# Optimization experiments

Measured on AMD Instinct MI355X. Metric: run time of the kernel, lower is better.

## Reference

```python
import jax, jax.numpy as jnp
import numpy as np

D_MODEL = 1024
HEADS = 4
HDIM = 64


def setup_inputs() -> dict:
    key = jax.random.key(0)
    k_x, k_qw, k_qb, k_kw, k_kb, k_hw = jax.random.split(key, 6)
    hidden_states = jax.random.normal(k_x, (2, 4096, D_MODEL), dtype=jnp.float32)
    # xavier_uniform bound for Linear(d_model -> heads*hdim)
    fan_out = HEADS * HDIM
    bound = float(np.sqrt(6.0 / (D_MODEL + fan_out)))
    q_weight = jax.random.uniform(k_qw, (fan_out, D_MODEL), minval=-bound, maxval=bound, dtype=jnp.float32)
    k_weight = jax.random.uniform(k_kw, (fan_out, D_MODEL), minval=-bound, maxval=bound, dtype=jnp.float32)
    # nn.Linear default bias init: U(-1/sqrt(fan_in), 1/sqrt(fan_in))
    b_bound = float(1.0 / np.sqrt(D_MODEL))
    q_bias = jax.random.uniform(k_qb, (fan_out,), minval=-b_bound, maxval=b_bound, dtype=jnp.float32)
    k_bias = jax.random.uniform(k_kb, (fan_out,), minval=-b_bound, maxval=b_bound, dtype=jnp.float32)
    indexer_weights = jax.random.normal(k_hw, (HEADS,), dtype=jnp.float32) * 0.1
    return {
        "hidden_states": hidden_states,
        "q_weight": q_weight,
        "q_bias": q_bias,
        "k_weight": k_weight,
        "k_bias": k_bias,
        "indexer_weights": indexer_weights,
    }


def reference(hidden_states, q_weight, q_bias, k_weight, k_bias, indexer_weights):
    b, s, _ = hidden_states.shape
    # Linear projections: x @ W^T + b  -> [b, s, heads*hdim]
    q = hidden_states @ q_weight.T + q_bias
    k = hidden_states @ k_weight.T + k_bias
    q = q.reshape(b, s, HEADS, HDIM)  # [b, s, h, d]
    k = k.reshape(b, s, HEADS, HDIM)
    # per-head QK^T -> [b, h, s, s]
    scores = jnp.einsum("bqhd,bkhd->bhqk", q, k)
    scores = jax.nn.relu(scores)
    # weighted sum over heads -> [b, s, s]
    index_scores = jnp.einsum("bhqk,h->bqk", scores, indexer_weights)
    return index_scores
```

## Files before the change

### kernel.cpp

```cpp
#include <hip/hip_runtime.h>


typedef __bf16 bf16;
typedef __bf16 bf16x4 __attribute__((ext_vector_type(4)));
typedef __bf16 bf16x8 __attribute__((ext_vector_type(8)));
typedef float f32x4 __attribute__((ext_vector_type(4)));

#define NB 2
#define SEQ 4096
#define DMODEL 1024
#define NHEAD 4
#define HDIM 64
#define NPROJ 256
#define MTOT 8192

__device__ __forceinline__ void async16(const void* g, void* l) {
  __builtin_amdgcn_global_load_lds(
      (const __attribute__((address_space(1))) void*)g,
      (__attribute__((address_space(3))) void*)l, 16, 0, 0);
}

__global__ __launch_bounds__(256) void k_convert(const float* __restrict__ wq,
                                                 const float* __restrict__ wk,
                                                 bf16* __restrict__ wqb,
                                                 bf16* __restrict__ wkb) {
  int i = blockIdx.x * 256 + threadIdx.x;
  float4 a = ((const float4*)wq)[i];
  bf16x4 oa = {(bf16)a.x, (bf16)a.y, (bf16)a.z, (bf16)a.w};
  ((bf16x4*)wqb)[i] = oa;
  float4 b = ((const float4*)wk)[i];
  bf16x4 ob = {(bf16)b.x, (bf16)b.y, (bf16)b.z, (bf16)b.w};
  ((bf16x4*)wkb)[i] = ob;
}

__global__ __launch_bounds__(256, 3) void k_proj(
    const float* __restrict__ x, const bf16* __restrict__ wqb,
    const bf16* __restrict__ wkb, const float* __restrict__ qbias,
    const float* __restrict__ kbias, bf16* __restrict__ Qb,
    bf16* __restrict__ Kb) {
  __shared__ __align__(16) bf16 As[64 * 72];
  __shared__ __align__(16) bf16 Bs[256 * 64];
  const int t = threadIdx.x;
  const int lane = t & 63, w = t >> 6;
  const int m16 = lane & 15, q = lane >> 4;
  const int m0 = blockIdx.x * 64;
  const int z = blockIdx.y;
  const bf16* W = z ? wkb : wqb;

  f32x4 acc[4][4];
#pragma unroll
  for (int i = 0; i < 4; i++)
#pragma unroll
    for (int j = 0; j < 4; j++) acc[i][j] = {0.f, 0.f, 0.f, 0.f};

  for (int kt = 0; kt < 16; kt++) {
#pragma unroll
    for (int p = 0; p < 8; p++) {
      int n0 = p * 32 + w * 8;
      int r = n0 + (lane >> 3);
      int c = (lane & 7) ^ (r & 7);
      async16(W + (size_t)r * DMODEL + kt * 64 + c * 8, Bs + n0 * 64);
    }
#pragma unroll
    for (int p = 0; p < 4; p++) {
      int r = p * 16 + (t >> 4);
      int c = (t & 15) * 4;
      float4 v = *(const float4*)(x + (size_t)(m0 + r) * DMODEL + kt * 64 + c);
      bf16x4 o = {(bf16)v.x, (bf16)v.y, (bf16)v.z, (bf16)v.w};
      *(bf16x4*)(As + r * 72 + c) = o;
    }
    __builtin_amdgcn_s_waitcnt(0);
    __syncthreads();

#pragma unroll
    for (int s = 0; s < 2; s++) {
      bf16x8 a[4], b[4];
#pragma unroll
      for (int mt = 0; mt < 4; mt++)
        a[mt] = *(const bf16x8*)(As + (mt * 16 + m16) * 72 + s * 32 + q * 8);
#pragma unroll
      for (int nt = 0; nt < 4; nt++) {
        int n = w * 64 + nt * 16 + m16;
        int cc = (4 * s + q) ^ (n & 7);
        b[nt] = *(const bf16x8*)(Bs + n * 64 + cc * 8);
      }
#pragma unroll
      for (int mt = 0; mt < 4; mt++)
#pragma unroll
        for (int nt = 0; nt < 4; nt++)
          acc[mt][nt] = __builtin_amdgcn_mfma_f32_16x16x32_bf16(
              a[mt], b[nt], acc[mt][nt], 0, 0, 0);
    }
    __syncthreads();
  }

  const float* bias = z ? kbias : qbias;
  bf16* outp = z ? Kb : Qb;
#pragma unroll
  for (int nt = 0; nt < 4; nt++) {
    int col = w * 64 + nt * 16 + m16;
    float bv = bias[col];
#pragma unroll
    for (int mt = 0; mt < 4; mt++) {
      int row0 = m0 + mt * 16 + q * 4;
#pragma unroll
      for (int e = 0; e < 4; e++)
        outp[(size_t)(row0 + e) * NPROJ + col] = (bf16)(acc[mt][nt][e] + bv);
    }
  }
}

__global__ __launch_bounds__(256, 2) void k_scores(
    const bf16* __restrict__ Qb, const bf16* __restrict__ Kb,
    const float* __restrict__ iw, float* __restrict__ out) {
  __shared__ __align__(16) bf16 Qs[128 * 64];
  __shared__ __align__(16) bf16 Ks[128 * 64];
  const int t = threadIdx.x;
  const int lane = t & 63, w = t >> 6;
  const int m16 = lane & 15, q = lane >> 4;
  const int kx = blockIdx.x, qy = blockIdx.y, bz = blockIdx.z;
  const int rh = (w >> 1) * 64, ch = (w & 1) * 64;

  f32x4 accf[4][4];
#pragma unroll
  for (int i = 0; i < 4; i++)
#pragma unroll
    for (int j = 0; j < 4; j++) accf[i][j] = {0.f, 0.f, 0.f, 0.f};

  const size_t qbase = ((size_t)bz * SEQ + (size_t)qy * 128) * NPROJ;
  const size_t kbase = ((size_t)bz * SEQ + (size_t)kx * 128) * NPROJ;

  for (int h = 0; h < NHEAD; h++) {
#pragma unroll
    for (int p = 0; p < 4; p++) {
      int r0 = w * 32 + p * 8;
      int r = r0 + (lane >> 3);
      int c = (lane & 7) ^ (r & 7);
      async16(Qb + qbase + (size_t)r * NPROJ + h * 64 + c * 8, Qs + r0 * 64);
      async16(Kb + kbase + (size_t)r * NPROJ + h * 64 + c * 8, Ks + r0 * 64);
    }
    __builtin_amdgcn_s_waitcnt(0);
    __syncthreads();

    float wh = iw[h];
    bf16x8 b0[4], b1[4];
#pragma unroll
    for (int nt = 0; nt < 4; nt++) {
      int n = ch + nt * 16 + m16;
      b0[nt] = *(const bf16x8*)(Ks + n * 64 + ((q) ^ (n & 7)) * 8);
      b1[nt] = *(const bf16x8*)(Ks + n * 64 + ((4 + q) ^ (n & 7)) * 8);
    }
#pragma unroll
    for (int mt = 0; mt < 4; mt++) {
      int m = rh + mt * 16 + m16;
      bf16x8 a0 = *(const bf16x8*)(Qs + m * 64 + ((q) ^ (m & 7)) * 8);
      bf16x8 a1 = *(const bf16x8*)(Qs + m * 64 + ((4 + q) ^ (m & 7)) * 8);
#pragma unroll
      for (int nt = 0; nt < 4; nt++) {
        f32x4 tacc = {0.f, 0.f, 0.f, 0.f};
        tacc = __builtin_amdgcn_mfma_f32_16x16x32_bf16(a0, b0[nt], tacc, 0, 0, 0);
        tacc = __builtin_amdgcn_mfma_f32_16x16x32_bf16(a1, b1[nt], tacc, 0, 0, 0);
#pragma unroll
        for (int e = 0; e < 4; e++)
          accf[mt][nt][e] += wh * fmaxf(tacc[e], 0.f);
      }
    }
    __syncthreads();
  }

#pragma unroll
  for (int mt = 0; mt < 4; mt++)
#pragma unroll
    for (int e = 0; e < 4; e++) {
      int row = qy * 128 + rh + mt * 16 + q * 4 + e;
      size_t ob = ((size_t)bz * SEQ + row) * SEQ + (size_t)kx * 128 + ch;
#pragma unroll
      for (int nt = 0; nt < 4; nt++)
        out[ob + nt * 16 + m16] = accf[mt][nt][e];
    }
}

extern "C" void kernel_launch(void* const* d_in, const int* in_sizes, int n_in,
                              void* d_out, int out_size, void* d_ws, size_t ws_size,
                              hipStream_t stream) {
  const float* x  = (const float*)d_in[0];
  const float* wq = (const float*)d_in[1];
  const float* qb = (const float*)d_in[2];
  const float* wk = (const float*)d_in[3];
  const float* kb = (const float*)d_in[4];
  const float* iw = (const float*)d_in[5];
  float* out = (float*)d_out;

  char* ws = (char*)d_ws;
  bf16* wqb = (bf16*)ws;
  bf16* wkb = (bf16*)(ws + 524288);
  bf16* Qb  = (bf16*)(ws + 1048576);
  bf16* Kb  = (bf16*)(ws + 1048576 + 4194304);

  k_convert<<<256, 256, 0, stream>>>(wq, wk, wqb, wkb);
  k_proj<<<dim3(128, 2, 1), 256, 0, stream>>>(x, wqb, wkb, qb, kb, Qb, Kb);
  k_scores<<<dim3(32, 32, 2), 256, 0, stream>>>(Qb, Kb, iw, out);
}
```

Measured before the change: 201.3 us.

## Drop LDS staging; load MFMA operands directly from global in proj and scores

Both the projection and the scores kernels stop staging tiles in shared memory and instead load MFMA fragments straight from global memory into registers, which removes the barriers and LDS traffic. The projection tile shrinks to 32 rows per block, giving twice as many blocks, and occupancy hints rise for both kernels. In exchange, operands that were shared across waves are now re-read by each wave through the caches, and loads are less coalesced.

```diff
diff --git a/kernel.cpp b/kernel.cpp
--- a/kernel.cpp
+++ b/kernel.cpp
@@ -14,12 +14,6 @@
 #define NPROJ 256
 #define MTOT 8192
 
-__device__ __forceinline__ void async16(const void* g, void* l) {
-  __builtin_amdgcn_global_load_lds(
-      (const __attribute__((address_space(1))) void*)g,
-      (__attribute__((address_space(3))) void*)l, 16, 0, 0);
-}
-
 __global__ __launch_bounds__(256) void k_convert(const float* __restrict__ wq,
                                                  const float* __restrict__ wk,
                                                  bf16* __restrict__ wqb,
@@ -33,75 +27,63 @@
   ((bf16x4*)wkb)[i] = ob;
 }
 
-__global__ __launch_bounds__(256, 3) void k_proj(
+__global__ __launch_bounds__(256, 4) void k_proj(
     const float* __restrict__ x, const bf16* __restrict__ wqb,
     const bf16* __restrict__ wkb, const float* __restrict__ qbias,
     const float* __restrict__ kbias, bf16* __restrict__ Qb,
     bf16* __restrict__ Kb) {
-  __shared__ __align__(16) bf16 As[64 * 72];
-  __shared__ __align__(16) bf16 Bs[256 * 64];
   const int t = threadIdx.x;
   const int lane = t & 63, w = t >> 6;
   const int m16 = lane & 15, q = lane >> 4;
-  const int m0 = blockIdx.x * 64;
+  const int m0 = blockIdx.x * 32;
   const int z = blockIdx.y;
-  const bf16* W = z ? wkb : wqb;
+  const bf16* __restrict__ W = z ? wkb : wqb;
 
-  f32x4 acc[4][4];
+  f32x4 acc[2][4];
 #pragma unroll
-  for (int i = 0; i < 4; i++)
+  for (int i = 0; i < 2; i++)
 #pragma unroll
     for (int j = 0; j < 4; j++) acc[i][j] = {0.f, 0.f, 0.f, 0.f};
 
+  const float* xp = x + (size_t)(m0 + m16) * DMODEL + q * 8;
+  const bf16* wp = W + (size_t)(w * 64 + m16) * DMODEL + q * 8;
+
   for (int kt = 0; kt < 16; kt++) {
+    bf16x8 a[2][2];
 #pragma unroll
-    for (int p = 0; p < 8; p++) {
-      int n0 = p * 32 + w * 8;
-      int r = n0 + (lane >> 3);
-      int c = (lane & 7) ^ (r & 7);
-      async16(W + (size_t)r * DMODEL + kt * 64 + c * 8, Bs + n0 * 64);
-    }
+    for (int mt = 0; mt < 2; mt++)
 #pragma unroll
-    for (int p = 0; p < 4; p++) {
-      int r = p * 16 + (t >> 4);
-      int c = (t & 15) * 4;
-      float4 v = *(const float4*)(x + (size_t)(m0 + r) * DMODEL + kt * 64 + c);
-      bf16x4 o = {(bf16)v.x, (bf16)v.y, (bf16)v.z, (bf16)v.w};
-      *(bf16x4*)(As + r * 72 + c) = o;
-    }
-    __builtin_amdgcn_s_waitcnt(0);
-    __syncthreads();
-
+      for (int s = 0; s < 2; s++) {
+        const float* p = xp + (size_t)mt * 16 * DMODEL + kt * 64 + s * 32;
+        float4 v0 = *(const float4*)p;
+        float4 v1 = *(const float4*)(p + 4);
+        a[mt][s] = bf16x8{(bf16)v0.x, (bf16)v0.y, (bf16)v0.z, (bf16)v0.w,
+                          (bf16)v1.x, (bf16)v1.y, (bf16)v1.z, (bf16)v1.w};
+      }
+    bf16x8 b[4][2];
 #pragma unroll
-    for (int s = 0; s < 2; s++) {
-      bf16x8 a[4], b[4];
+    for (int nt = 0; nt < 4; nt++)
 #pragma unroll
-      for (int mt = 0; mt < 4; mt++)
-        a[mt] = *(const bf16x8*)(As + (mt * 16 + m16) * 72 + s * 32 + q * 8);
+      for (int s = 0; s < 2; s++)
+        b[nt][s] = *(const bf16x8*)(wp + (size_t)nt * 16 * DMODEL + kt * 64 + s * 32);
 #pragma unroll
-      for (int nt = 0; nt < 4; nt++) {
-        int n = w * 64 + nt * 16 + m16;
-        int cc = (4 * s + q) ^ (n & 7);
-        b[nt] = *(const bf16x8*)(Bs + n * 64 + cc * 8);
-      }
+    for (int mt = 0; mt < 2; mt++)
 #pragma unroll
-      for (int mt = 0; mt < 4; mt++)
+      for (int nt = 0; nt < 4; nt++)
 #pragma unroll
-        for (int nt = 0; nt < 4; nt++)
+        for (int s = 0; s < 2; s++)
           acc[mt][nt] = __builtin_amdgcn_mfma_f32_16x16x32_bf16(
-              a[mt], b[nt], acc[mt][nt], 0, 0, 0);
-    }
-    __syncthreads();
+              a[mt][s], b[nt][s], acc[mt][nt], 0, 0, 0);
   }
 
-  const float* bias = z ? kbias : qbias;
-  bf16* outp = z ? Kb : Qb;
+  const float* __restrict__ bias = z ? kbias : qbias;
+  bf16* __restrict__ outp = z ? Kb : Qb;
 #pragma unroll
   for (int nt = 0; nt < 4; nt++) {
     int col = w * 64 + nt * 16 + m16;
     float bv = bias[col];
 #pragma unroll
-    for (int mt = 0; mt < 4; mt++) {
+    for (int mt = 0; mt < 2; mt++) {
       int row0 = m0 + mt * 16 + q * 4;
 #pragma unroll
       for (int e = 0; e < 4; e++)
@@ -110,11 +92,9 @@
   }
 }
 
-__global__ __launch_bounds__(256, 2) void k_scores(
+__global__ __launch_bounds__(256, 3) void k_scores(
     const bf16* __restrict__ Qb, const bf16* __restrict__ Kb,
     const float* __restrict__ iw, float* __restrict__ out) {
-  __shared__ __align__(16) bf16 Qs[128 * 64];
-  __shared__ __align__(16) bf16 Ks[128 * 64];
   const int t = threadIdx.x;
   const int lane = t & 63, w = t >> 6;
   const int m16 = lane & 15, q = lane >> 4;
@@ -127,45 +107,36 @@
 #pragma unroll
     for (int j = 0; j < 4; j++) accf[i][j] = {0.f, 0.f, 0.f, 0.f};
 
-  const size_t qbase = ((size_t)bz * SEQ + (size_t)qy * 128) * NPROJ;
-  const size_t kbase = ((size_t)bz * SEQ + (size_t)kx * 128) * NPROJ;
+  const float w0 = iw[0], w1 = iw[1], w2 = iw[2], w3 = iw[3];
+  const float whs[4] = {w0, w1, w2, w3};
+
+  const bf16* qp = Qb + (size_t)(bz * SEQ + qy * 128 + rh + m16) * NPROJ + q * 8;
+  const bf16* kp = Kb + (size_t)(bz * SEQ + kx * 128 + ch + m16) * NPROJ + q * 8;
 
   for (int h = 0; h < NHEAD; h++) {
+    const int ho = h * 64;
+    bf16x8 a0[4], a1[4], b0[4], b1[4];
 #pragma unroll
-    for (int p = 0; p < 4; p++) {
-      int r0 = w * 32 + p * 8;
-      int r = r0 + (lane >> 3);
-      int c = (lane & 7) ^ (r & 7);
-      async16(Qb + qbase + (size_t)r * NPROJ + h * 64 + c * 8, Qs + r0 * 64);
-      async16(Kb + kbase + (size_t)r * NPROJ + h * 64 + c * 8, Ks + r0 * 64);
+    for (int i = 0; i < 4; i++) {
+      const bf16* qpi = qp + (size_t)i * 16 * NPROJ + ho;
+      a0[i] = *(const bf16x8*)(qpi);
+      a1[i] = *(const bf16x8*)(qpi + 32);
+      const bf16* kpi = kp + (size_t)i * 16 * NPROJ + ho;
+      b0[i] = *(const bf16x8*)(kpi);
+      b1[i] = *(const bf16x8*)(kpi + 32);
     }
-    __builtin_amdgcn_s_waitcnt(0);
-    __syncthreads();
-
-    float wh = iw[h];
-    bf16x8 b0[4], b1[4];
+    float wh = whs[h];
 #pragma unroll
-    for (int nt = 0; nt < 4; nt++) {
-      int n = ch + nt * 16 + m16;
-      b0[nt] = *(const bf16x8*)(Ks + n * 64 + ((q) ^ (n & 7)) * 8);
-      b1[nt] = *(const bf16x8*)(Ks + n * 64 + ((4 + q) ^ (n & 7)) * 8);
-    }
-#pragma unroll
-    for (int mt = 0; mt < 4; mt++) {
-      int m = rh + mt * 16 + m16;
-      bf16x8 a0 = *(const bf16x8*)(Qs + m * 64 + ((q) ^ (m & 7)) * 8);
-      bf16x8 a1 = *(const bf16x8*)(Qs + m * 64 + ((4 + q) ^ (m & 7)) * 8);
+    for (int mt = 0; mt < 4; mt++)
 #pragma unroll
       for (int nt = 0; nt < 4; nt++) {
         f32x4 tacc = {0.f, 0.f, 0.f, 0.f};
-        tacc = __builtin_amdgcn_mfma_f32_16x16x32_bf16(a0, b0[nt], tacc, 0, 0, 0);
-        tacc = __builtin_amdgcn_mfma_f32_16x16x32_bf16(a1, b1[nt], tacc, 0, 0, 0);
+        tacc = __builtin_amdgcn_mfma_f32_16x16x32_bf16(a0[mt], b0[nt], tacc, 0, 0, 0);
+        tacc = __builtin_amdgcn_mfma_f32_16x16x32_bf16(a1[mt], b1[nt], tacc, 0, 0, 0);
 #pragma unroll
         for (int e = 0; e < 4; e++)
           accf[mt][nt][e] += wh * fmaxf(tacc[e], 0.f);
       }
-    }
-    __syncthreads();
   }
 
 #pragma unroll
@@ -198,6 +169,6 @@
   bf16* Kb  = (bf16*)(ws + 1048576 + 4194304);
 
   k_convert<<<256, 256, 0, stream>>>(wq, wk, wqb, wkb);
-  k_proj<<<dim3(128, 2, 1), 256, 0, stream>>>(x, wqb, wkb, qb, kb, Qb, Kb);
+  k_proj<<<dim3(256, 2, 1), 256, 0, stream>>>(x, wqb, wkb, qb, kb, Qb, Kb);
   k_scores<<<dim3(32, 32, 2), 256, 0, stream>>>(Qb, Kb, iw, out);
 }
```

Measured after the change: 267.2 us. 1.33x slower.

## Split projection N across blocks, load two heads per stage, XCD-aware score tiling

Applied to the files above, without the earlier changes.

The projection kernel now splits the 256 output columns into two 128-column halves via a third grid dimension. This doubles the block count to improve occupancy and cuts B-tile LDS, at the cost of converting the x tile to bf16 twice. The scores kernel loads two heads per LDS stage, halving the number of barriers and load rounds. It also remaps a flat 2048-block grid so that blocks on the same XCD share query rows, which should improve L2 reuse of Q tiles.

```diff
diff --git a/kernel.cpp b/kernel.cpp
--- a/kernel.cpp
+++ b/kernel.cpp
@@ -33,33 +33,35 @@
   ((bf16x4*)wkb)[i] = ob;
 }
 
-__global__ __launch_bounds__(256, 3) void k_proj(
+__global__ __launch_bounds__(256, 4) void k_proj(
     const float* __restrict__ x, const bf16* __restrict__ wqb,
     const bf16* __restrict__ wkb, const float* __restrict__ qbias,
     const float* __restrict__ kbias, bf16* __restrict__ Qb,
     bf16* __restrict__ Kb) {
   __shared__ __align__(16) bf16 As[64 * 72];
-  __shared__ __align__(16) bf16 Bs[256 * 64];
+  __shared__ __align__(16) bf16 Bs[128 * 64];
   const int t = threadIdx.x;
   const int lane = t & 63, w = t >> 6;
   const int m16 = lane & 15, q = lane >> 4;
   const int m0 = blockIdx.x * 64;
   const int z = blockIdx.y;
-  const bf16* W = z ? wkb : wqb;
-
-  f32x4 acc[4][4];
+  const int nh = blockIdx.z;
+  const bf16* __restrict__ W = z ? wkb : wqb;
+
+  f32x4 acc[4][2];
 #pragma unroll
   for (int i = 0; i < 4; i++)
 #pragma unroll
-    for (int j = 0; j < 4; j++) acc[i][j] = {0.f, 0.f, 0.f, 0.f};
+    for (int j = 0; j < 2; j++) acc[i][j] = {0.f, 0.f, 0.f, 0.f};
 
   for (int kt = 0; kt < 16; kt++) {
 #pragma unroll
-    for (int p = 0; p < 8; p++) {
-      int n0 = p * 32 + w * 8;
+    for (int p = 0; p < 4; p++) {
+      int n0 = w * 32 + p * 8;
       int r = n0 + (lane >> 3);
       int c = (lane & 7) ^ (r & 7);
-      async16(W + (size_t)r * DMODEL + kt * 64 + c * 8, Bs + n0 * 64);
+      async16(W + (size_t)(nh * 128 + r) * DMODEL + kt * 64 + c * 8,
+              Bs + n0 * 64);
     }
 #pragma unroll
     for (int p = 0; p < 4; p++) {
@@ -74,31 +76,31 @@
 
 #pragma unroll
     for (int s = 0; s < 2; s++) {
-      bf16x8 a[4], b[4];
+      bf16x8 a[4], b[2];
 #pragma unroll
       for (int mt = 0; mt < 4; mt++)
         a[mt] = *(const bf16x8*)(As + (mt * 16 + m16) * 72 + s * 32 + q * 8);
 #pragma unroll
-      for (int nt = 0; nt < 4; nt++) {
-        int n = w * 64 + nt * 16 + m16;
+      for (int nt = 0; nt < 2; nt++) {
+        int n = w * 32 + nt * 16 + m16;
         int cc = (4 * s + q) ^ (n & 7);
         b[nt] = *(const bf16x8*)(Bs + n * 64 + cc * 8);
       }
 #pragma unroll
       for (int mt = 0; mt < 4; mt++)
 #pragma unroll
-        for (int nt = 0; nt < 4; nt++)
+        for (int nt = 0; nt < 2; nt++)
           acc[mt][nt] = __builtin_amdgcn_mfma_f32_16x16x32_bf16(
               a[mt], b[nt], acc[mt][nt], 0, 0, 0);
     }
     __syncthreads();
   }
 
-  const float* bias = z ? kbias : qbias;
-  bf16* outp = z ? Kb : Qb;
-#pragma unroll
-  for (int nt = 0; nt < 4; nt++) {
-    int col = w * 64 + nt * 16 + m16;
+  const float* __restrict__ bias = z ? kbias : qbias;
+  bf16* __restrict__ outp = z ? Kb : Qb;
+#pragma unroll
+  for (int nt = 0; nt < 2; nt++) {
+    int col = nh * 128 + w * 32 + nt * 16 + m16;
     float bv = bias[col];
 #pragma unroll
     for (int mt = 0; mt < 4; mt++) {
@@ -113,12 +115,20 @@
 __global__ __launch_bounds__(256, 2) void k_scores(
     const bf16* __restrict__ Qb, const bf16* __restrict__ Kb,
     const float* __restrict__ iw, float* __restrict__ out) {
-  __shared__ __align__(16) bf16 Qs[128 * 64];
-  __shared__ __align__(16) bf16 Ks[128 * 64];
+  __shared__ __align__(16) bf16 Qs[16 * 2 * 512];
+  __shared__ __align__(16) bf16 Ks[16 * 2 * 512];
   const int t = threadIdx.x;
   const int lane = t & 63, w = t >> 6;
   const int m16 = lane & 15, q = lane >> 4;
-  const int kx = blockIdx.x, qy = blockIdx.y, bz = blockIdx.z;
+
+  const int L = blockIdx.x;
+  const int xcd = L & 7;
+  const int slot = L >> 3;
+  const int row = xcd * 8 + (slot >> 5);
+  const int kx = slot & 31;
+  const int bz = row >> 5;
+  const int qy = row & 31;
+
   const int rh = (w >> 1) * 64, ch = (w & 1) * 64;
 
   f32x4 accf[4][4];
@@ -130,40 +140,47 @@
   const size_t qbase = ((size_t)bz * SEQ + (size_t)qy * 128) * NPROJ;
   const size_t kbase = ((size_t)bz * SEQ + (size_t)kx * 128) * NPROJ;
 
-  for (int h = 0; h < NHEAD; h++) {
-#pragma unroll
-    for (int p = 0; p < 4; p++) {
-      int r0 = w * 32 + p * 8;
-      int r = r0 + (lane >> 3);
+  for (int hp = 0; hp < 2; hp++) {
+#pragma unroll
+    for (int p = 0; p < 8; p++) {
+      int idx = w * 8 + p;
+      int g = idx >> 1, hh = idx & 1;
+      int r = g * 8 + (lane >> 3);
       int c = (lane & 7) ^ (r & 7);
-      async16(Qb + qbase + (size_t)r * NPROJ + h * 64 + c * 8, Qs + r0 * 64);
-      async16(Kb + kbase + (size_t)r * NPROJ + h * 64 + c * 8, Ks + r0 * 64);
+      size_t src = (size_t)r * NPROJ + (hp * 2 + hh) * 64 + c * 8;
+      async16(Qb + qbase + src, Qs + idx * 512);
+      async16(Kb + kbase + src, Ks + idx * 512);
     }
     __builtin_amdgcn_s_waitcnt(0);
     __syncthreads();
 
-    float wh = iw[h];
-    bf16x8 b0[4], b1[4];
-#pragma unroll
-    for (int nt = 0; nt < 4; nt++) {
-      int n = ch + nt * 16 + m16;
-      b0[nt] = *(const bf16x8*)(Ks + n * 64 + ((q) ^ (n & 7)) * 8);
-      b1[nt] = *(const bf16x8*)(Ks + n * 64 + ((4 + q) ^ (n & 7)) * 8);
-    }
-#pragma unroll
-    for (int mt = 0; mt < 4; mt++) {
-      int m = rh + mt * 16 + m16;
-      bf16x8 a0 = *(const bf16x8*)(Qs + m * 64 + ((q) ^ (m & 7)) * 8);
-      bf16x8 a1 = *(const bf16x8*)(Qs + m * 64 + ((4 + q) ^ (m & 7)) * 8);
+#pragma unroll
+    for (int hh = 0; hh < 2; hh++) {
+      float wh = iw[hp * 2 + hh];
+      bf16x8 b0[4], b1[4];
 #pragma unroll
       for (int nt = 0; nt < 4; nt++) {
-        f32x4 tacc = {0.f, 0.f, 0.f, 0.f};
-        tacc = __builtin_amdgcn_mfma_f32_16x16x32_bf16(a0, b0[nt], tacc, 0, 0, 0);
-        tacc = __builtin_amdgcn_mfma_f32_16x16x32_bf16(a1, b1[nt], tacc, 0, 0, 0);
-#pragma unroll
-        for (int e = 0; e < 4; e++)
-          accf[mt][nt][e] += wh * fmaxf(tacc[e], 0.f);
+        int n = ch + nt * 16 + m16;
+        const bf16* kb_ = Ks + (n >> 3) * 1024 + hh * 512 + (n & 7) * 64;
+        b0[nt] = *(const bf16x8*)(kb_ + ((q) ^ (n & 7)) * 8);
+        b1[nt] = *(const bf16x8*)(kb_ + ((4 + q) ^ (n & 7)) * 8);
       }
+#pragma unroll
+      for (int mt = 0; mt < 4; mt++) {
+        int m = rh + mt * 16 + m16;
+        const bf16* qa = Qs + (m >> 3) * 1024 + hh * 512 + (m & 7) * 64;
+        bf16x8 a0 = *(const bf16x8*)(qa + ((q) ^ (m & 7)) * 8);
+        bf16x8 a1 = *(const bf16x8*)(qa + ((4 + q) ^ (m & 7)) * 8);
+#pragma unroll
+        for (int nt = 0; nt < 4; nt++) {
+          f32x4 tacc = {0.f, 0.f, 0.f, 0.f};
+          tacc = __builtin_amdgcn_mfma_f32_16x16x32_bf16(a0, b0[nt], tacc, 0, 0, 0);
+          tacc = __builtin_amdgcn_mfma_f32_16x16x32_bf16(a1, b1[nt], tacc, 0, 0, 0);
+#pragma unroll
+          for (int e = 0; e < 4; e++)
+            accf[mt][nt][e] += wh * fmaxf(tacc[e], 0.f);
+        }
+      }
     }
     __syncthreads();
   }
@@ -172,8 +189,8 @@
   for (int mt = 0; mt < 4; mt++)
 #pragma unroll
     for (int e = 0; e < 4; e++) {
-      int row = qy * 128 + rh + mt * 16 + q * 4 + e;
-      size_t ob = ((size_t)bz * SEQ + row) * SEQ + (size_t)kx * 128 + ch;
+      int r = qy * 128 + rh + mt * 16 + q * 4 + e;
+      size_t ob = ((size_t)bz * SEQ + r) * SEQ + (size_t)kx * 128 + ch;
 #pragma unroll
       for (int nt = 0; nt < 4; nt++)
         out[ob + nt * 16 + m16] = accf[mt][nt][e];
@@ -198,6 +215,6 @@
   bf16* Kb  = (bf16*)(ws + 1048576 + 4194304);
 
   k_convert<<<256, 256, 0, stream>>>(wq, wk, wqb, wkb);
-  k_proj<<<dim3(128, 2, 1), 256, 0, stream>>>(x, wqb, wkb, qb, kb, Qb, Kb);
-  k_scores<<<dim3(32, 32, 2), 256, 0, stream>>>(Qb, Kb, iw, out);
-}
+  k_proj<<<dim3(128, 2, 2), 256, 0, stream>>>(x, wqb, wkb, qb, kb, Qb, Kb);
+  k_scores<<<2048, 256, 0, stream>>>(Qb, Kb, iw, out);
+}
```

After: 202.6 us. No clear change (+0.6%).
